# Performance work log

Hardware: AMD Instinct MI355X
Metric: run time of the kernel (lower is better)

Reference implementation:

```python
import jax, jax.numpy as jnp
import numpy as np

B, N, D = 64, 512, 3
COORD_W, EDGE_W, COUNT_W = 1.0, 1.0, 0.1
EPS = 1e-7


def setup_inputs() -> dict:
    key = jax.random.key(0)
    k0, k1, k2, k3, k4, k5 = jax.random.split(key, 6)
    predicted_coords = jax.random.normal(k0, (B, N, D), dtype=jnp.float32)
    points = jax.random.normal(k1, (B, N, D), dtype=jnp.float32)
    # predicted adjacency probabilities strictly inside (0, 1) for BCE
    adjacency_matrix = jax.random.uniform(k2, (B, N, N), dtype=jnp.float32,
                                          minval=1e-6, maxval=1.0 - 1e-6)
    adjacency = (jax.random.uniform(k3, (B, N, N)) < 0.1).astype(jnp.float32)
    # ragged prefix node masks (module slices [:n_actual], so masks are contiguous prefixes)
    lengths = jax.random.randint(k4, (B,), 1, N + 1)
    node_masks = (jnp.arange(N)[None, :] < lengths[:, None]).astype(jnp.int32)
    # predicted node counts near the true counts
    node_counts = lengths.astype(jnp.float32)[:, None] + jax.random.normal(k5, (B, 1), dtype=jnp.float32) * 5.0
    return {
        'predicted_coords': predicted_coords,
        'adjacency_matrix': adjacency_matrix,
        'node_counts': node_counts,
        'points': points,
        'adjacency': adjacency,
        'node_masks': node_masks,
    }


def reference(predicted_coords, adjacency_matrix, node_counts, points, adjacency, node_masks):
    m = node_masks.astype(predicted_coords.dtype)            # [B, N] prefix mask
    n = m.sum(axis=1)                                        # [B] nodes per sample
    d = predicted_coords.shape[-1]

    # per-sample mean-squared coordinate error over the first n_b nodes
    se = ((predicted_coords - points) ** 2 * m[:, :, None]).sum(axis=(1, 2))  # [B]
    coord_b = se / jnp.maximum(n * d, 1.0)

    # per-sample BCE over the n_b x n_b adjacency block
    m2 = m[:, :, None] * m[:, None, :]                       # [B, N, N]
    p = jnp.clip(adjacency_matrix, EPS, 1.0 - EPS)
    bce = -(adjacency * jnp.log(p) + (1.0 - adjacency) * jnp.log1p(-p))
    edge_b = (bce * m2).sum(axis=(1, 2)) / jnp.maximum(n * n, 1.0)

    valid = (n > 0).astype(coord_b.dtype)                    # [B]
    vc = valid.sum()
    denom = jnp.maximum(vc, 1.0)
    coord_loss = jnp.where(vc > 0, (coord_b * valid).sum() / denom, 0.0)
    edge_loss = jnp.where(vc > 0, (edge_b * valid).sum() / denom, 0.0)

    predicted_counts = node_counts.squeeze()
    predicted_counts = jnp.atleast_1d(predicted_counts)
    count_loss = jnp.mean((predicted_counts - n) ** 2)

    total_loss = COORD_W * coord_loss + EDGE_W * edge_loss + COUNT_W * count_loss
    return (total_loss, coord_loss, edge_loss, count_loss)
```

## Files before the change

kernel.cpp:

```cpp
#include <hip/hip_runtime.h>

#define BB 64
#define NN 512
#define DD 3
#define EPSF 1e-7f
#define SPLIT 64

#define WS_EDGE 0
#define WS_N    (BB * SPLIT)
#define WS_SE   (BB * SPLIT + BB)

__global__ __launch_bounds__(256) void fused_kernel(const float* __restrict__ am,
                                                    const float* __restrict__ adj,
                                                    const float* __restrict__ pc,
                                                    const float* __restrict__ pts,
                                                    const int* __restrict__ masks,
                                                    float* __restrict__ ws) {
    const int bx  = blockIdx.x;
    const int b   = blockIdx.y;
    const int tid = threadIdx.x;

    __shared__ int   s_n;
    __shared__ float s_part[4];
    __shared__ float s_cpart[4];

    const int2 mv = ((const int2*)(masks + b * NN))[tid];
    const int  nxt = (tid < 255) ? masks[b * NN + 2 * tid + 2] : 0;
    if (tid == 0 && mv.x == 0) s_n = 0;
    if (mv.x == 1 && mv.y == 0) s_n = 2 * tid + 1;
    if (mv.y == 1 && nxt == 0)  s_n = 2 * tid + 2;
    __syncthreads();
    const int n = s_n;

    const int wid  = tid >> 6;
    const int lane = tid & 63;

    if (bx == 0) {
        const float* pcb = pc  + b * (NN * DD);
        const float* ptb = pts + b * (NN * DD);
        float se = 0.f;
        for (int e = tid; e < NN * DD; e += 256) {
            if (e < n * DD) {
                const float d = pcb[e] - ptb[e];
                se += d * d;
            }
        }
#pragma unroll
        for (int off = 32; off; off >>= 1) se += __shfl_xor(se, off);
        if (lane == 0) s_cpart[wid] = se;
    }

    const int half    = tid >> 7;
    const int lane128 = tid & 127;
    const int j0      = lane128 * 4;
    float sum = 0.f;
    if (j0 < n) {
        const size_t bbase = (size_t)b * NN * NN;
        for (int row = bx + half * SPLIT; row < n; row += 2 * SPLIT) {
            const float4 p4 = *(const float4*)(am  + bbase + (size_t)row * NN + j0);
            const float4 a4 = *(const float4*)(adj + bbase + (size_t)row * NN + j0);
            const float pv[4] = {p4.x, p4.y, p4.z, p4.w};
            const float av[4] = {a4.x, a4.y, a4.z, a4.w};
#pragma unroll
            for (int k = 0; k < 4; ++k) {
                if (j0 + k < n) {
                    const float p = fminf(fmaxf(pv[k], EPSF), 1.f - EPSF);
                    const float q = (av[k] != 0.f) ? p : (1.f - p);
                    sum -= __logf(q);
                }
            }
        }
    }
#pragma unroll
    for (int off = 32; off; off >>= 1) sum += __shfl_xor(sum, off);
    if (lane == 0) s_part[wid] = sum;
    __syncthreads();

    if (tid == 0) {
        ws[WS_EDGE + b * SPLIT + bx] = s_part[0] + s_part[1] + s_part[2] + s_part[3];
        if (bx == 0) {
            ws[WS_N + b]  = (float)n;
            ws[WS_SE + b] = s_cpart[0] + s_cpart[1] + s_cpart[2] + s_cpart[3];
        }
    }
}

__global__ __launch_bounds__(64) void final_kernel(const float* __restrict__ ws,
                                                   const float* __restrict__ counts,
                                                   float* __restrict__ out) {
    const int b = threadIdx.x;

    const float4* ep = (const float4*)(ws + WS_EDGE + b * SPLIT);
    float es = 0.f;
#pragma unroll
    for (int k = 0; k < SPLIT / 4; ++k) {
        const float4 v = ep[k];
        es += v.x + v.y + v.z + v.w;
    }

    const float n  = ws[WS_N + b];
    const float se = ws[WS_SE + b];

    const float coord_b = se / fmaxf(n * (float)DD, 1.f);
    const float edge_b  = es / fmaxf(n * n, 1.f);
    const float valid   = (n > 0.f) ? 1.f : 0.f;
    const float dc      = counts[b] - n;

    float v0 = valid;
    float v1 = coord_b * valid;
    float v2 = edge_b * valid;
    float v3 = dc * dc;
    for (int off = 32; off > 0; off >>= 1) {
        v0 += __shfl_down(v0, off);
        v1 += __shfl_down(v1, off);
        v2 += __shfl_down(v2, off);
        v3 += __shfl_down(v3, off);
    }
    if (b == 0) {
        const float vc = v0;
        const float denom = fmaxf(vc, 1.f);
        const float coord_loss = (vc > 0.f) ? (v1 / denom) : 0.f;
        const float edge_loss  = (vc > 0.f) ? (v2 / denom) : 0.f;
        const float count_loss = v3 / (float)BB;
        out[0] = coord_loss + edge_loss + 0.1f * count_loss;
        out[1] = coord_loss;
        out[2] = edge_loss;
        out[3] = count_loss;
    }
}

extern "C" void kernel_launch(void* const* d_in, const int* in_sizes, int n_in,
                              void* d_out, int out_size, void* d_ws, size_t ws_size,
                              hipStream_t stream) {
    const float* pc    = (const float*)d_in[0];
    const float* am    = (const float*)d_in[1];
    const float* nc    = (const float*)d_in[2];
    const float* pts   = (const float*)d_in[3];
    const float* adj   = (const float*)d_in[4];
    const int*   masks = (const int*)d_in[5];
    float* ws  = (float*)d_ws;
    float* out = (float*)d_out;

    dim3 grid(SPLIT, BB);
    fused_kernel<<<grid, 256, 0, stream>>>(am, adj, pc, pts, masks, ws);
    final_kernel<<<1, 64, 0, stream>>>(ws, nc, out);
}
```

Measured before the change: 21.48 us.

## Prefetch first row before mask sync, count mask via ballot, halve block split

Measured after the change: 21.54 us. Within noise of the previous version (+0.3%).

```diff
diff --git a/kernel.cpp b/kernel.cpp
--- a/kernel.cpp
+++ b/kernel.cpp
@@ -4,11 +4,12 @@
 #define NN 512
 #define DD 3
 #define EPSF 1e-7f
-#define SPLIT 64
+#define SPLIT 32
+#define NBLK (BB * SPLIT)
 
 #define WS_EDGE 0
-#define WS_N    (BB * SPLIT)
-#define WS_SE   (BB * SPLIT + BB)
+#define WS_N    NBLK
+#define WS_SE   (NBLK + BB)
 
 __global__ __launch_bounds__(256) void fused_kernel(const float* __restrict__ am,
                                                     const float* __restrict__ adj,
@@ -19,21 +20,27 @@
     const int bx  = blockIdx.x;
     const int b   = blockIdx.y;
     const int tid = threadIdx.x;
+    const int wid  = tid >> 6;
+    const int lane = tid & 63;
+    const int half    = tid >> 7;
+    const int lane128 = tid & 127;
+    const int j0      = lane128 * 4;
 
-    __shared__ int   s_n;
+    __shared__ int   s_cnt4[4];
     __shared__ float s_part[4];
     __shared__ float s_cpart[4];
 
+    const size_t bbase = (size_t)b * NN * NN;
+    const int row0 = bx + half * SPLIT;
+    const float4 p0 = *(const float4*)(am  + bbase + (size_t)row0 * NN + j0);
+    const float4 a0 = *(const float4*)(adj + bbase + (size_t)row0 * NN + j0);
+
     const int2 mv = ((const int2*)(masks + b * NN))[tid];
-    const int  nxt = (tid < 255) ? masks[b * NN + 2 * tid + 2] : 0;
-    if (tid == 0 && mv.x == 0) s_n = 0;
-    if (mv.x == 1 && mv.y == 0) s_n = 2 * tid + 1;
-    if (mv.y == 1 && nxt == 0)  s_n = 2 * tid + 2;
+    const unsigned long long bl0 = __ballot(mv.x != 0);
+    const unsigned long long bl1 = __ballot(mv.y != 0);
+    if (lane == 0) s_cnt4[wid] = __popcll(bl0) + __popcll(bl1);
     __syncthreads();
-    const int n = s_n;
-
-    const int wid  = tid >> 6;
-    const int lane = tid & 63;
+    const int n = s_cnt4[0] + s_cnt4[1] + s_cnt4[2] + s_cnt4[3];
 
     if (bx == 0) {
         const float* pcb = pc  + b * (NN * DD);
@@ -50,13 +57,22 @@
         if (lane == 0) s_cpart[wid] = se;
     }
 
-    const int half    = tid >> 7;
-    const int lane128 = tid & 127;
-    const int j0      = lane128 * 4;
     float sum = 0.f;
+    if (row0 < n && j0 < n) {
+        const float pv[4] = {p0.x, p0.y, p0.z, p0.w};
+        const float av[4] = {a0.x, a0.y, a0.z, a0.w};
+#pragma unroll
+        for (int k = 0; k < 4; ++k) {
+            if (j0 + k < n) {
+                const float r = (av[k] != 0.f) ? pv[k] : 1.f - pv[k];
+                const float q = fminf(fmaxf(r, EPSF), 1.f - EPSF);
+                sum -= __logf(q);
+            }
+        }
+    }
     if (j0 < n) {
-        const size_t bbase = (size_t)b * NN * NN;
-        for (int row = bx + half * SPLIT; row < n; row += 2 * SPLIT) {
+#pragma unroll 2
+        for (int row = row0 + 2 * SPLIT; row < n; row += 2 * SPLIT) {
             const float4 p4 = *(const float4*)(am  + bbase + (size_t)row * NN + j0);
             const float4 a4 = *(const float4*)(adj + bbase + (size_t)row * NN + j0);
             const float pv[4] = {p4.x, p4.y, p4.z, p4.w};
@@ -64,8 +80,8 @@
 #pragma unroll
             for (int k = 0; k < 4; ++k) {
                 if (j0 + k < n) {
-                    const float p = fminf(fmaxf(pv[k], EPSF), 1.f - EPSF);
-                    const float q = (av[k] != 0.f) ? p : (1.f - p);
+                    const float r = (av[k] != 0.f) ? pv[k] : 1.f - pv[k];
+                    const float q = fminf(fmaxf(r, EPSF), 1.f - EPSF);
                     sum -= __logf(q);
                 }
             }
@@ -110,6 +126,7 @@
     float v1 = coord_b * valid;
     float v2 = edge_b * valid;
     float v3 = dc * dc;
+#pragma unroll
     for (int off = 32; off > 0; off >>= 1) {
         v0 += __shfl_down(v0, off);
         v1 += __shfl_down(v1, off);
```

## Assign one wave per adjacency row and multiply probabilities before taking logs

Applied to the files above, without the earlier changes.

After: 27.60 us. 1.29x slower.

```diff
diff --git a/kernel.cpp b/kernel.cpp
--- a/kernel.cpp
+++ b/kernel.cpp
@@ -4,11 +4,14 @@
 #define NN 512
 #define DD 3
 #define EPSF 1e-7f
-#define SPLIT 64
+#define NBLOCK 2048
+#define NWAVE (NBLOCK * 4)
+#define TOTROWS (BB * NN)
+#define TSTEPS (TOTROWS / NWAVE)
 
 #define WS_EDGE 0
-#define WS_N    (BB * SPLIT)
-#define WS_SE   (BB * SPLIT + BB)
+#define WS_N    TOTROWS
+#define WS_SE   (TOTROWS + BB)
 
 __global__ __launch_bounds__(256) void fused_kernel(const float* __restrict__ am,
                                                     const float* __restrict__ adj,
@@ -16,107 +19,125 @@
                                                     const float* __restrict__ pts,
                                                     const int* __restrict__ masks,
                                                     float* __restrict__ ws) {
-    const int bx  = blockIdx.x;
-    const int b   = blockIdx.y;
-    const int tid = threadIdx.x;
+    const int tid  = threadIdx.x;
+    const int lane = tid & 63;
+    const int gw   = blockIdx.x * 4 + (tid >> 6);
+    const int j0   = lane * 8;
 
-    __shared__ int   s_n;
-    __shared__ float s_part[4];
-    __shared__ float s_cpart[4];
+    if (gw < BB) {
+        const int s = gw;
+        const int4 cA = *(const int4*)(masks + s * NN + j0);
+        const int4 cB = *(const int4*)(masks + s * NN + j0 + 4);
+        const int  cm[8] = {cA.x, cA.y, cA.z, cA.w, cB.x, cB.y, cB.z, cB.w};
+        const float4* pv4 = (const float4*)(pc  + s * (NN * DD) + j0 * DD);
+        const float4* tv4 = (const float4*)(pts + s * (NN * DD) + j0 * DD);
+        float pe[24], te[24];
+#pragma unroll
+        for (int q = 0; q < 6; ++q) {
+            const float4 a = pv4[q], b = tv4[q];
+            pe[4*q] = a.x; pe[4*q+1] = a.y; pe[4*q+2] = a.z; pe[4*q+3] = a.w;
+            te[4*q] = b.x; te[4*q+1] = b.y; te[4*q+2] = b.z; te[4*q+3] = b.w;
+        }
+        float se = 0.f;
+#pragma unroll
+        for (int k = 0; k < 24; ++k) {
+            if (cm[k / 3]) { const float d = pe[k] - te[k]; se += d * d; }
+        }
+#pragma unroll
+        for (int off = 32; off; off >>= 1) se += __shfl_xor(se, off);
+        if (lane == 0) ws[WS_SE + s] = se;
+    } else if (gw < 2 * BB) {
+        const int s = gw - BB;
+        const int4 cA = *(const int4*)(masks + s * NN + j0);
+        const int4 cB = *(const int4*)(masks + s * NN + j0 + 4);
+        int cnt = cA.x + cA.y + cA.z + cA.w + cB.x + cB.y + cB.z + cB.w;
+#pragma unroll
+        for (int off = 32; off; off >>= 1) cnt += __shfl_xor(cnt, off);
+        if (lane == 0) ws[WS_N + s] = (float)cnt;
+    }
 
-    const int2 mv = ((const int2*)(masks + b * NN))[tid];
-    const int  nxt = (tid < 255) ? masks[b * NN + 2 * tid + 2] : 0;
-    if (tid == 0 && mv.x == 0) s_n = 0;
-    if (mv.x == 1 && mv.y == 0) s_n = 2 * tid + 1;
-    if (mv.y == 1 && nxt == 0)  s_n = 2 * tid + 2;
-    __syncthreads();
-    const int n = s_n;
-
-    const int wid  = tid >> 6;
-    const int lane = tid & 63;
-
-    if (bx == 0) {
-        const float* pcb = pc  + b * (NN * DD);
-        const float* ptb = pts + b * (NN * DD);
-        float se = 0.f;
-        for (int e = tid; e < NN * DD; e += 256) {
-            if (e < n * DD) {
-                const float d = pcb[e] - ptb[e];
-                se += d * d;
+#pragma unroll
+    for (int t = 0; t < TSTEPS; ++t) {
+        const int R = gw + NWAVE * t;
+        float sum = 0.f;
+        if (masks[R] != 0) {
+            const int  b    = R >> 9;
+            const int* mk   = masks + b * NN;
+            const size_t base = (size_t)R * NN;
+            const int m_lo = mk[j0];
+            if (m_lo) {
+                const int m_hi = mk[j0 + 7];
+                const float4 p0 = *(const float4*)(am  + base + j0);
+                const float4 p1 = *(const float4*)(am  + base + j0 + 4);
+                const float4 a0 = *(const float4*)(adj + base + j0);
+                const float4 a1 = *(const float4*)(adj + base + j0 + 4);
+                const float pv[8] = {p0.x, p0.y, p0.z, p0.w, p1.x, p1.y, p1.z, p1.w};
+                const float av[8] = {a0.x, a0.y, a0.z, a0.w, a1.x, a1.y, a1.z, a1.w};
+                float prod0 = 1.f, prod1 = 1.f;
+                if (m_hi) {
+#pragma unroll
+                    for (int k = 0; k < 4; ++k) {
+                        float r = (av[k] != 0.f) ? pv[k] : 1.f - pv[k];
+                        prod0 *= fminf(fmaxf(r, EPSF), 1.f - EPSF);
+                        r = (av[k+4] != 0.f) ? pv[k+4] : 1.f - pv[k+4];
+                        prod1 *= fminf(fmaxf(r, EPSF), 1.f - EPSF);
+                    }
+                } else {
+                    const int4 mA = *(const int4*)(mk + j0);
+                    const int4 mB = *(const int4*)(mk + j0 + 4);
+                    const int mv[8] = {mA.x, mA.y, mA.z, mA.w, mB.x, mB.y, mB.z, mB.w};
+#pragma unroll
+                    for (int k = 0; k < 4; ++k) {
+                        float r = (av[k] != 0.f) ? pv[k] : 1.f - pv[k];
+                        float q = fminf(fmaxf(r, EPSF), 1.f - EPSF);
+                        prod0 *= mv[k] ? q : 1.f;
+                        r = (av[k+4] != 0.f) ? pv[k+4] : 1.f - pv[k+4];
+                        q = fminf(fmaxf(r, EPSF), 1.f - EPSF);
+                        prod1 *= mv[k+4] ? q : 1.f;
+                    }
+                }
+                sum = -(__logf(prod0) + __logf(prod1));
             }
         }
 #pragma unroll
-        for (int off = 32; off; off >>= 1) se += __shfl_xor(se, off);
-        if (lane == 0) s_cpart[wid] = se;
-    }
-
-    const int half    = tid >> 7;
-    const int lane128 = tid & 127;
-    const int j0      = lane128 * 4;
-    float sum = 0.f;
-    if (j0 < n) {
-        const size_t bbase = (size_t)b * NN * NN;
-        for (int row = bx + half * SPLIT; row < n; row += 2 * SPLIT) {
-            const float4 p4 = *(const float4*)(am  + bbase + (size_t)row * NN + j0);
-            const float4 a4 = *(const float4*)(adj + bbase + (size_t)row * NN + j0);
-            const float pv[4] = {p4.x, p4.y, p4.z, p4.w};
-            const float av[4] = {a4.x, a4.y, a4.z, a4.w};
-#pragma unroll
-            for (int k = 0; k < 4; ++k) {
-                if (j0 + k < n) {
-                    const float p = fminf(fmaxf(pv[k], EPSF), 1.f - EPSF);
-                    const float q = (av[k] != 0.f) ? p : (1.f - p);
-                    sum -= __logf(q);
-                }
-            }
-        }
-    }
-#pragma unroll
-    for (int off = 32; off; off >>= 1) sum += __shfl_xor(sum, off);
-    if (lane == 0) s_part[wid] = sum;
-    __syncthreads();
-
-    if (tid == 0) {
-        ws[WS_EDGE + b * SPLIT + bx] = s_part[0] + s_part[1] + s_part[2] + s_part[3];
-        if (bx == 0) {
-            ws[WS_N + b]  = (float)n;
-            ws[WS_SE + b] = s_cpart[0] + s_cpart[1] + s_cpart[2] + s_cpart[3];
-        }
+        for (int off = 32; off; off >>= 1) sum += __shfl_xor(sum, off);
+        if (lane == 0) ws[WS_EDGE + t * NWAVE + gw] = sum;
     }
 }
 
 __global__ __launch_bounds__(64) void final_kernel(const float* __restrict__ ws,
                                                    const float* __restrict__ counts,
                                                    float* __restrict__ out) {
-    const int b = threadIdx.x;
+    const int s = threadIdx.x;
 
-    const float4* ep = (const float4*)(ws + WS_EDGE + b * SPLIT);
+    const float4* ep = (const float4*)(ws + WS_EDGE + (s >> 4) * NWAVE + (s & 15) * NN);
     float es = 0.f;
 #pragma unroll
-    for (int k = 0; k < SPLIT / 4; ++k) {
+    for (int k = 0; k < NN / 4; ++k) {
         const float4 v = ep[k];
         es += v.x + v.y + v.z + v.w;
     }
 
-    const float n  = ws[WS_N + b];
-    const float se = ws[WS_SE + b];
+    const float n  = ws[WS_N + s];
+    const float se = ws[WS_SE + s];
 
     const float coord_b = se / fmaxf(n * (float)DD, 1.f);
     const float edge_b  = es / fmaxf(n * n, 1.f);
     const float valid   = (n > 0.f) ? 1.f : 0.f;
-    const float dc      = counts[b] - n;
+    const float dc      = counts[s] - n;
 
     float v0 = valid;
     float v1 = coord_b * valid;
     float v2 = edge_b * valid;
     float v3 = dc * dc;
+#pragma unroll
     for (int off = 32; off > 0; off >>= 1) {
         v0 += __shfl_down(v0, off);
         v1 += __shfl_down(v1, off);
         v2 += __shfl_down(v2, off);
         v3 += __shfl_down(v3, off);
     }
-    if (b == 0) {
+    if (s == 0) {
         const float vc = v0;
         const float denom = fmaxf(vc, 1.f);
         const float coord_loss = (vc > 0.f) ? (v1 / denom) : 0.f;
@@ -141,7 +162,6 @@
     float* ws  = (float*)d_ws;
     float* out = (float*)d_out;
 
-    dim3 grid(SPLIT, BB);
-    fused_kernel<<<grid, 256, 0, stream>>>(am, adj, pc, pts, masks, ws);
+    fused_kernel<<<NBLOCK, 256, 0, stream>>>(am, adj, pc, pts, masks, ws);
     final_kernel<<<1, 64, 0, stream>>>(ws, nc, out);
 }
```
